# Kernel tuning notes

Hardware: AMD Instinct MI355X
Metric: run time of the kernel (lower is better)

The kernel has to match this reference:

```python
import jax, jax.numpy as jnp
import numpy as np

D_H = 2048      # d_hidden
D_E = 1408      # d_expert (per routed expert)
E = 8           # n_routed_experts
K = 2           # n_experts_per_token (top-k)
N_SHARED = 2    # n_shared_experts -> shared expert dim = D_E * N_SHARED
B, S = 1, 2048
D_S = D_E * N_SHARED


def setup_inputs() -> dict:
    key = jax.random.key(0)
    ks = jax.random.split(key, 8)
    def init(k, shape, fan_in):
        # nn.Linear default init: U(-1/sqrt(fan_in), 1/sqrt(fan_in))
        bound = 1.0 / np.sqrt(fan_in)
        return jax.random.uniform(k, shape, jnp.float32, -bound, bound)
    x = jax.random.normal(ks[0], (B, S, D_H), jnp.float32)
    gate_W = init(ks[1], (E, D_H), D_H)          # router: logits = x @ gate_W.T
    Wg_e = init(ks[2], (E, D_E, D_H), D_H)       # per-expert W_gate (out,in)
    Wu_e = init(ks[3], (E, D_E, D_H), D_H)       # per-expert W_up
    Wd_e = init(ks[4], (E, D_H, D_E), D_E)       # per-expert W_down
    Wg_s = init(ks[5], (D_S, D_H), D_H)          # shared expert W_gate
    Wu_s = init(ks[6], (D_S, D_H), D_H)
    Wd_s = init(ks[7], (D_H, D_S), D_S)
    return {"x": x, "gate_W": gate_W, "Wg_e": Wg_e, "Wu_e": Wu_e,
            "Wd_e": Wd_e, "Wg_s": Wg_s, "Wu_s": Wu_s, "Wd_s": Wd_s}


def reference(x, gate_W, Wg_e, Wu_e, Wd_e, Wg_s, Wu_s, Wd_s):
    silu = jax.nn.silu
    # shared expert: SiLU-gated MLP over all tokens
    shared = (silu(x @ Wg_s.T) * (x @ Wu_s.T)) @ Wd_s.T          # [B,S,D_H]
    # gating: softmax over experts, then top-k scores/indices
    scores = jax.nn.softmax(x @ gate_W.T, axis=-1)                # [B,S,E]
    topk_scores, topk_idx = jax.lax.top_k(scores, K)              # [B,S,K]
    # dense combine weights w[t,e] = topk score if e selected else 0
    # (equivalent to the torch argsort-dispatch + scatter_reduce sum combine)
    w = jnp.sum(jax.nn.one_hot(topk_idx, E, dtype=x.dtype) * topk_scores[..., None], axis=-2)  # [B,S,E]
    xf = x.reshape(-1, D_H)                                       # [T,D_H], T = B*S
    wf = w.reshape(-1, E)                                         # [T,E]
    # per-expert SiLU-gated MLP, batched over experts
    g = jnp.einsum('td,efd->etf', xf, Wg_e)                       # [E,T,D_E]
    u = jnp.einsum('td,efd->etf', xf, Wu_e)
    h = silu(g) * u
    oe = jnp.einsum('etf,edf->etd', h, Wd_e)                      # [E,T,D_H]
    routed = jnp.einsum('etd,te->td', oe, wf).reshape(B, S, D_H)
    return routed + shared
```

## Files before the change

kernel.cpp:

```cpp
#include <hip/hip_runtime.h>

using short8 = __attribute__((ext_vector_type(8))) short;
using f32x4  = __attribute__((ext_vector_type(4))) float;
typedef unsigned short ushort_t;
typedef unsigned int u32;

#define T_TOK 2048
#define DH 2048
#define DE 1408
#define DS 2816
#define NB_GU 800
#define NB_DN 896

#define NGEc 23068672UL
#define NGSc 5767168UL
#define NXc  4194304UL
#define PA_CVT_BLOCKS 30208
#define PB_CVT_BLOCKS 14080

__device__ __forceinline__ unsigned short f2bf(float f) {
  unsigned u = __float_as_uint(f);
  u += 0x7FFF + ((u >> 16) & 1);
  return (unsigned short)(u >> 16);
}

__device__ __forceinline__ void gl_lds16(const void* g, void* l) {
  __builtin_amdgcn_global_load_lds((const __attribute__((address_space(1))) u32*)g,
                                   (__attribute__((address_space(3))) u32*)l, 16, 0, 0);
}

__device__ __forceinline__ short8 pack_bf8(float4 a, float4 b) {
  short8 o;
  o[0] = (short)f2bf(a.x); o[1] = (short)f2bf(a.y);
  o[2] = (short)f2bf(a.z); o[3] = (short)f2bf(a.w);
  o[4] = (short)f2bf(b.x); o[5] = (short)f2bf(b.y);
  o[6] = (short)f2bf(b.z); o[7] = (short)f2bf(b.w);
  return o;
}

__global__ void phaseA_kernel(const float* __restrict__ x, const float* __restrict__ gW,
                              int* __restrict__ counts, int* __restrict__ tok_e,
                              int* __restrict__ tok_slot, float* __restrict__ tok_w,
                              const float* __restrict__ Wg_e, const float* __restrict__ Wu_e,
                              const float* __restrict__ Wg_s, const float* __restrict__ Wu_s,
                              ushort_t* wbg_e, ushort_t* wbu_e,
                              ushort_t* wbg_s, ushort_t* wbu_s, ushort_t* xb) {
  int b = blockIdx.x;
  int tid = threadIdx.x;
  if (b < 512) {
    int wid = tid >> 6, lane = tid & 63;
    int t = b * 4 + wid;
    float acc[8] = {0.f,0.f,0.f,0.f,0.f,0.f,0.f,0.f};
    const float* xt = x + (size_t)t * DH;
    for (int i = lane; i < DH; i += 64) {
      float xv = xt[i];
#pragma unroll
      for (int e = 0; e < 8; e++) acc[e] += xv * gW[e * DH + i];
    }
#pragma unroll
    for (int e = 0; e < 8; e++) {
#pragma unroll
      for (int off = 32; off > 0; off >>= 1) acc[e] += __shfl_xor(acc[e], off);
    }
    if (lane == 0) {
      float mx = acc[0];
      for (int e = 1; e < 8; e++) mx = fmaxf(mx, acc[e]);
      float p[8], se = 0.f;
      for (int e = 0; e < 8; e++) { p[e] = __expf(acc[e] - mx); se += p[e]; }
      for (int e = 0; e < 8; e++) p[e] /= se;
      int i1 = 0;
      for (int e = 1; e < 8; e++) if (p[e] > p[i1]) i1 = e;
      int i2 = (i1 == 0) ? 1 : 0;
      for (int e = 0; e < 8; e++) if (e != i1 && p[e] > p[i2]) i2 = e;
      int s1 = atomicAdd(&counts[i1], 1);
      int s2 = atomicAdd(&counts[i2], 1);
      tok_e[2 * t] = i1;     tok_e[2 * t + 1] = i2;
      tok_slot[2 * t] = s1;  tok_slot[2 * t + 1] = s2;
      tok_w[2 * t] = p[i1];  tok_w[2 * t + 1] = p[i2];
    }
    return;
  }
  size_t i = (size_t)(b - 512) * 2048 + (size_t)tid * 8;
  const float* s; ushort_t* d; size_t o;
  if      (i < NGEc)                    { s = Wg_e; d = wbg_e; o = i; }
  else if (i < 2 * NGEc)                { s = Wu_e; d = wbu_e; o = i - NGEc; }
  else if (i < 2 * NGEc + NGSc)         { s = Wg_s; d = wbg_s; o = i - 2 * NGEc; }
  else if (i < 2 * NGEc + 2 * NGSc)     { s = Wu_s; d = wbu_s; o = i - 2 * NGEc - NGSc; }
  else                                  { s = x;    d = xb;    o = i - 2 * NGEc - 2 * NGSc; }
  float4 a = *(const float4*)(s + o);
  float4 bb = *(const float4*)(s + o + 4);
  *(short8*)(d + o) = pack_bf8(a, bb);
}

__global__ void prefix_assign_kernel(const int* __restrict__ counts, int* __restrict__ ebase,
                                     int* __restrict__ gu_off, int* __restrict__ dn_off,
                                     const int* __restrict__ tok_e, int* __restrict__ tok_slot,
                                     int* __restrict__ slot2tok) {
  __shared__ int sbase[8];
  if (threadIdx.x == 0) {
    int a = 0;
    for (int e = 0; e < 8; e++) { sbase[e] = a; ebase[e] = a; a += counts[e]; }
    int g = 0, d = 0;
    for (int z = 0; z < 8; z++) {
      gu_off[z] = g; dn_off[z] = d;
      int L = (counts[z] + 127) >> 7;
      g += L * 11; d += L * 16;
    }
    gu_off[8] = g; g += 176;
    gu_off[9] = g; g += 176;
    gu_off[10] = g;
    dn_off[8] = d; d += 256;
    dn_off[9] = d;
  }
  __syncthreads();
  for (int idx = threadIdx.x; idx < T_TOK * 2; idx += blockDim.x) {
    int e = tok_e[idx];
    int g = sbase[e] + tok_slot[idx];
    tok_slot[idx] = g;
    slot2tok[g] = idx >> 1;
  }
}

#define GU_BK 32
#define GU_OP 8192
#define GU_BUF 24576
__global__ __launch_bounds__(256, 2) void phaseB_kernel(
    const ushort_t* __restrict__ xb, const int* __restrict__ counts,
    const int* __restrict__ ebase, const int* __restrict__ gu_off,
    const int* __restrict__ slot2tok,
    const ushort_t* __restrict__ Wbg_e, const ushort_t* __restrict__ Wbu_e,
    const ushort_t* __restrict__ Wbg_s, const ushort_t* __restrict__ Wbu_s,
    ushort_t* __restrict__ h_r, ushort_t* __restrict__ h_s,
    const float* __restrict__ Wd_e, const float* __restrict__ Wd_s,
    ushort_t* wbd_e, ushort_t* wbd_s) {
  __shared__ char smem[2 * GU_BUF];
  int tid = threadIdx.x;
  if (blockIdx.x >= NB_GU) {
    size_t i = (size_t)(blockIdx.x - NB_GU) * 2048 + (size_t)tid * 8;
    const float* s; ushort_t* d; size_t o;
    if (i < NGEc) { s = Wd_e; d = wbd_e; o = i; }
    else          { s = Wd_s; d = wbd_s; o = i - NGEc; }
    float4 a = *(const float4*)(s + o);
    float4 bb = *(const float4*)(s + o + 4);
    *(short8*)(d + o) = pack_bf8(a, bb);
    return;
  }
  int b = blockIdx.x;
  int c = (b & 7) * (NB_GU >> 3) + (b >> 3);
  int off[11];
#pragma unroll
  for (int zz = 0; zz < 11; zz++) off[zz] = gu_off[zz];
  if (c >= off[10]) return;
  int z = 0;
#pragma unroll
  for (int zz = 1; zz < 10; zz++) if (c >= off[zz]) z = zz;
  int cz = c - off[z];

  bool routed = (z < 8);
  int cnt, gbase, Lm;
  const ushort_t *Bg, *Bu;
  if (routed) {
    cnt = counts[z]; gbase = ebase[z];
    Lm = (cnt + 127) >> 7;
    Bg = Wbg_e + (size_t)z * DE * DH;
    Bu = Wbu_e + (size_t)z * DE * DH;
  } else {
    cnt = T_TOK; gbase = 0; Lm = 16;
    Bg = Wbg_s + (size_t)(z - 8) * 1408 * DH;
    Bu = Wbu_s + (size_t)(z - 8) * 1408 * DH;
  }
  int mt = cz % Lm, y = cz / Lm;
  int m0 = mt * 128, n0 = y * 128;

  int lane = tid & 63, w = tid >> 6;
  int lr = lane & 15, lk = lane >> 4;
  int wr = w >> 1, wc = w & 1;

  const ushort_t* asrc[2];
  const ushort_t* gsrc[2];
  const ushort_t* usrc[2];
  int dst[2];
#pragma unroll
  for (int j = 0; j < 2; j++) {
    int r = (w * 2 + j) * 16 + (lane >> 2);
    int lrow = m0 + r;
    int tok = routed ? ((lrow < cnt) ? slot2tok[gbase + lrow] : 0) : lrow;
    int cs = (lane & 3) ^ ((r >> 1) & 3);
    asrc[j] = xb + (size_t)tok * DH + cs * 8;
    gsrc[j] = Bg + (size_t)(n0 + r) * DH + cs * 8;
    usrc[j] = Bu + (size_t)(n0 + r) * DH + cs * 8;
    dst[j] = (w * 2 + j) * 1024;
  }

  f32x4 accg[4][4] = {};
  f32x4 accu[4][4] = {};

#define GU_STAGE(buf, k0)                                              \
  {                                                                    \
    char* bb = smem + (buf) * GU_BUF;                                  \
    _Pragma("unroll")                                                  \
    for (int j = 0; j < 2; j++) {                                      \
      gl_lds16(asrc[j] + (k0), bb + dst[j]);                           \
      gl_lds16(gsrc[j] + (k0), bb + GU_OP + dst[j]);                   \
      gl_lds16(usrc[j] + (k0), bb + 2 * GU_OP + dst[j]);               \
    }                                                                  \
  }

  GU_STAGE(0, 0);
  __syncthreads();
  int cur = 0;
  for (int kc = 0; kc < DH; kc += GU_BK) {
    if (kc + GU_BK < DH) GU_STAGE(cur ^ 1, kc + GU_BK);
    const char* bb = smem + cur * GU_BUF;
    short8 af[4], bg[4], bu[4];
#pragma unroll
    for (int m = 0; m < 4; m++) {
      int rr = wr * 64 + m * 16 + lr;
      af[m] = *(const short8*)(bb + rr * 64 + ((lk ^ ((rr >> 1) & 3)) << 4));
    }
#pragma unroll
    for (int n = 0; n < 4; n++) {
      int cc = wc * 64 + n * 16 + lr;
      bg[n] = *(const short8*)(bb + GU_OP + cc * 64 + ((lk ^ ((cc >> 1) & 3)) << 4));
      bu[n] = *(const short8*)(bb + 2 * GU_OP + cc * 64 + ((lk ^ ((cc >> 1) & 3)) << 4));
    }
#pragma unroll
    for (int m = 0; m < 4; m++) {
#pragma unroll
      for (int n = 0; n < 4; n++) {
        accg[m][n] = __builtin_amdgcn_mfma_f32_16x16x32_bf16(af[m], bg[n], accg[m][n], 0, 0, 0);
        accu[m][n] = __builtin_amdgcn_mfma_f32_16x16x32_bf16(af[m], bu[n], accu[m][n], 0, 0, 0);
      }
    }
    __syncthreads();
    cur ^= 1;
  }
#pragma unroll
  for (int m = 0; m < 4; m++) {
    int rowl = m0 + wr * 64 + m * 16 + lk * 4;
#pragma unroll
    for (int n = 0; n < 4; n++) {
      int col = n0 + wc * 64 + n * 16 + lr;
#pragma unroll
      for (int j = 0; j < 4; j++) {
        float g = accg[m][n][j], u = accu[m][n][j];
        float s = g / (1.f + __expf(-g));
        unsigned short hv = f2bf(s * u);
        if (routed) {
          if (rowl + j < cnt) h_r[(size_t)(gbase + rowl + j) * DE + col] = hv;
        } else {
          h_s[(size_t)(rowl + j) * DS + (z - 8) * 1408 + col] = hv;
        }
      }
    }
  }
}

#define DN_BK 32
#define DN_OP 8192
#define DN_BUF 16384
__global__ __launch_bounds__(256, 3) void down_kernel(
    const ushort_t* __restrict__ h_r, const ushort_t* __restrict__ h_s,
    const int* __restrict__ counts, const int* __restrict__ ebase,
    const int* __restrict__ dn_off,
    const ushort_t* __restrict__ Wbd_e, const ushort_t* __restrict__ Wbd_s,
    float* __restrict__ oe, float* __restrict__ out) {
  __shared__ char smem[3 * DN_BUF];

  int b = blockIdx.x;
  int c = (b & 7) * (NB_DN >> 3) + (b >> 3);
  int off[10];
#pragma unroll
  for (int zz = 0; zz < 10; zz++) off[zz] = dn_off[zz];
  if (c >= off[9]) return;
  int z = 0;
#pragma unroll
  for (int zz = 1; zz < 9; zz++) if (c >= off[zz]) z = zz;
  int cz = c - off[z];

  bool routed = (z < 8);
  int cnt, gbase, K, Lm;
  const ushort_t* Abase;
  const ushort_t* B;
  if (routed) {
    cnt = counts[z]; gbase = ebase[z];
    Lm = (cnt + 127) >> 7;
    K = DE;
    Abase = h_r + (size_t)gbase * DE;
    B = Wbd_e + (size_t)z * DH * DE;
  } else {
    cnt = T_TOK; gbase = 0; Lm = 16;
    K = DS;
    Abase = h_s;
    B = Wbd_s;
  }
  int mt = cz % Lm, y = cz / Lm;
  int m0 = mt * 128, n0 = y * 128;

  int tid = threadIdx.x;
  int lane = tid & 63, w = tid >> 6;
  int lr = lane & 15, lk = lane >> 4;
  int wr = w >> 1, wc = w & 1;

  const ushort_t* asrc[2];
  const ushort_t* bsrc[2];
  int dst[2];
#pragma unroll
  for (int j = 0; j < 2; j++) {
    int r = (w * 2 + j) * 16 + (lane >> 2);
    int cs = (lane & 3) ^ ((r >> 1) & 3);
    asrc[j] = Abase + (size_t)(m0 + r) * K + cs * 8;
    bsrc[j] = B + (size_t)(n0 + r) * K + cs * 8;
    dst[j] = (w * 2 + j) * 1024;
  }

  f32x4 acc[4][4] = {};

#define DN_STAGE(sbuf, k0)                                            \
  {                                                                   \
    char* bb = smem + (sbuf) * DN_BUF;                                \
    _Pragma("unroll")                                                 \
    for (int j = 0; j < 2; j++) {                                     \
      gl_lds16(asrc[j] + (k0), bb + dst[j]);                          \
      gl_lds16(bsrc[j] + (k0), bb + DN_OP + dst[j]);                  \
    }                                                                 \
  }

  const int NT = K / DN_BK;
  DN_STAGE(0, 0);
  DN_STAGE(1, DN_BK);
  int cur = 0;
  for (int i = 0; i < NT; i++) {
    if (i + 1 < NT) asm volatile("s_waitcnt vmcnt(4)" ::: "memory");
    else            asm volatile("s_waitcnt vmcnt(0)" ::: "memory");
    __builtin_amdgcn_s_barrier();
    asm volatile("" ::: "memory");
    if (i + 2 < NT) {
      int s2 = cur + 2; if (s2 >= 3) s2 -= 3;
      DN_STAGE(s2, (i + 2) * DN_BK);
    }
    const char* bb = smem + cur * DN_BUF;
    short8 af[4], bf[4];
#pragma unroll
    for (int m = 0; m < 4; m++) {
      int rr = wr * 64 + m * 16 + lr;
      af[m] = *(const short8*)(bb + rr * 64 + ((lk ^ ((rr >> 1) & 3)) << 4));
    }
#pragma unroll
    for (int n = 0; n < 4; n++) {
      int cc = wc * 64 + n * 16 + lr;
      bf[n] = *(const short8*)(bb + DN_OP + cc * 64 + ((lk ^ ((cc >> 1) & 3)) << 4));
    }
#pragma unroll
    for (int m = 0; m < 4; m++) {
#pragma unroll
      for (int n = 0; n < 4; n++) {
        acc[m][n] = __builtin_amdgcn_mfma_f32_16x16x32_bf16(af[m], bf[n], acc[m][n], 0, 0, 0);
      }
    }
    cur = (cur + 1 >= 3) ? 0 : cur + 1;
  }
#pragma unroll
  for (int m = 0; m < 4; m++) {
    int rowl = m0 + wr * 64 + m * 16 + lk * 4;
#pragma unroll
    for (int n = 0; n < 4; n++) {
      int col = n0 + wc * 64 + n * 16 + lr;
#pragma unroll
      for (int j = 0; j < 4; j++) {
        if (routed) {
          if (rowl + j < cnt) oe[(size_t)(gbase + rowl + j) * DH + col] = acc[m][n][j];
        } else {
          out[(size_t)(rowl + j) * DH + col] = acc[m][n][j];
        }
      }
    }
  }
}

__global__ void combine_kernel(const int* __restrict__ tok_gslot,
                               const float* __restrict__ tok_w,
                               const float* __restrict__ oe,
                               float* __restrict__ out) {
  int t = blockIdx.x;
  int g1 = tok_gslot[2 * t], g2 = tok_gslot[2 * t + 1];
  float w1 = tok_w[2 * t], w2 = tok_w[2 * t + 1];
  int i = threadIdx.x * 8;
  const float4* p1 = (const float4*)(oe + (size_t)g1 * DH + i);
  const float4* p2 = (const float4*)(oe + (size_t)g2 * DH + i);
  float4* po = (float4*)(out + (size_t)t * DH + i);
  float4 a0 = p1[0], a1 = p1[1];
  float4 b0 = p2[0], b1 = p2[1];
  float4 o0 = po[0], o1 = po[1];
  o0.x += w1 * a0.x + w2 * b0.x;  o0.y += w1 * a0.y + w2 * b0.y;
  o0.z += w1 * a0.z + w2 * b0.z;  o0.w += w1 * a0.w + w2 * b0.w;
  o1.x += w1 * a1.x + w2 * b1.x;  o1.y += w1 * a1.y + w2 * b1.y;
  o1.z += w1 * a1.z + w2 * b1.z;  o1.w += w1 * a1.w + w2 * b1.w;
  po[0] = o0; po[1] = o1;
}

extern "C" void kernel_launch(void* const* d_in, const int* in_sizes, int n_in,
                              void* d_out, int out_size, void* d_ws, size_t ws_size,
                              hipStream_t stream) {
  const float* x    = (const float*)d_in[0];
  const float* gW   = (const float*)d_in[1];
  const float* Wg_e = (const float*)d_in[2];
  const float* Wu_e = (const float*)d_in[3];
  const float* Wd_e = (const float*)d_in[4];
  const float* Wg_s = (const float*)d_in[5];
  const float* Wu_s = (const float*)d_in[6];
  const float* Wd_s = (const float*)d_in[7];
  float* out = (float*)d_out;

  char* ws = (char*)d_ws;
  int*   counts   = (int*)ws;
  int*   ebase    = (int*)(ws + 64);
  int*   gu_off   = (int*)(ws + 128);
  int*   dn_off   = (int*)(ws + 192);
  int*   tok_e    = (int*)(ws + 256);
  int*   tok_slot = (int*)(ws + 256 + 16384);
  float* tok_w    = (float*)(ws + 256 + 32768);
  int*   slot2tok = (int*)(ws + 256 + 49152);
  ushort_t* xb  = (ushort_t*)(ws + 131072);
  ushort_t* h_r = (ushort_t*)(ws + 131072 + (size_t)T_TOK * DH * 2);
  ushort_t* h_s = h_r + (size_t)4096 * DE;
  float*    oe  = (float*)((char*)h_s + (size_t)T_TOK * DS * 2);
  ushort_t* wb  = (ushort_t*)((char*)oe + (size_t)4096 * DH * 4);
  ushort_t* wbg_e = wb;
  ushort_t* wbu_e = wb + NGEc;
  ushort_t* wbd_e = wb + 2 * NGEc;
  ushort_t* wbg_s = wb + 3 * NGEc;
  ushort_t* wbu_s = wbg_s + NGSc;
  ushort_t* wbd_s = wbg_s + 2 * NGSc;

  hipMemsetAsync(counts, 0, 64, stream);
  phaseA_kernel<<<512 + PA_CVT_BLOCKS, 256, 0, stream>>>(
      x, gW, counts, tok_e, tok_slot, tok_w,
      Wg_e, Wu_e, Wg_s, Wu_s, wbg_e, wbu_e, wbg_s, wbu_s, xb);
  prefix_assign_kernel<<<1, 256, 0, stream>>>(counts, ebase, gu_off, dn_off,
                                              tok_e, tok_slot, slot2tok);
  phaseB_kernel<<<NB_GU + PB_CVT_BLOCKS, 256, 0, stream>>>(
      xb, counts, ebase, gu_off, slot2tok, wbg_e, wbu_e, wbg_s, wbu_s, h_r, h_s,
      Wd_e, Wd_s, wbd_e, wbd_s);
  down_kernel<<<NB_DN, 256, 0, stream>>>(
      h_r, h_s, counts, ebase, dn_off, wbd_e, wbd_s, oe, out);
  combine_kernel<<<T_TOK, 256, 0, stream>>>(tok_slot, tok_w, oe, out);
}
```

Before: 389.1 us.

## Enlarge down-projection tiles to 256x256 with 512-thread blocks and BK=64

The down-projection GEMM moves from 128x128 tiles with 256 threads and a triple-buffered BK=32 pipeline to 256x256 tiles with 512 threads, BK=64 double buffering in 128KB of dynamic LDS, and an XOR swizzle. The tile schedule in prefix_assign is updated to match, and the grid drops to 256 blocks, about one per CU. The goal is higher operand reuse and less global traffic per FLOP. In exchange, occupancy falls to one block per CU, padding waste on routed experts grows, and a full barrier is taken each K step.

```diff
diff --git a/kernel.cpp b/kernel.cpp
--- a/kernel.cpp
+++ b/kernel.cpp
@@ -10,11 +10,10 @@
 #define DE 1408
 #define DS 2816
 #define NB_GU 800
-#define NB_DN 896
+#define DN_NB 256
 
 #define NGEc 23068672UL
 #define NGSc 5767168UL
-#define NXc  4194304UL
 #define PA_CVT_BLOCKS 30208
 #define PB_CVT_BLOCKS 14080
 
@@ -104,12 +103,14 @@
     for (int z = 0; z < 8; z++) {
       gu_off[z] = g; dn_off[z] = d;
       int L = (counts[z] + 127) >> 7;
-      g += L * 11; d += L * 16;
+      g += L * 11;
+      int Ld = (counts[z] + 255) >> 8;
+      d += Ld * 8;
     }
     gu_off[8] = g; g += 176;
     gu_off[9] = g; g += 176;
     gu_off[10] = g;
-    dn_off[8] = d; d += 256;
+    dn_off[8] = d; d += 64;
     dn_off[9] = d;
   }
   __syncthreads();
@@ -256,19 +257,16 @@
   }
 }
 
-#define DN_BK 32
-#define DN_OP 8192
-#define DN_BUF 16384
-__global__ __launch_bounds__(256, 3) void down_kernel(
+__global__ __launch_bounds__(512, 1) void down_kernel(
     const ushort_t* __restrict__ h_r, const ushort_t* __restrict__ h_s,
     const int* __restrict__ counts, const int* __restrict__ ebase,
     const int* __restrict__ dn_off,
     const ushort_t* __restrict__ Wbd_e, const ushort_t* __restrict__ Wbd_s,
     float* __restrict__ oe, float* __restrict__ out) {
-  __shared__ char smem[3 * DN_BUF];
+  extern __shared__ char smem[];
 
   int b = blockIdx.x;
-  int c = (b & 7) * (NB_DN >> 3) + (b >> 3);
+  int c = (b & 7) * (DN_NB >> 3) + (b >> 3);
   int off[10];
 #pragma unroll
   for (int zz = 0; zz < 10; zz++) off[zz] = dn_off[zz];
@@ -281,91 +279,103 @@
   bool routed = (z < 8);
   int cnt, gbase, K, Lm;
   const ushort_t* Abase;
-  const ushort_t* B;
+  const ushort_t* Bw;
   if (routed) {
     cnt = counts[z]; gbase = ebase[z];
-    Lm = (cnt + 127) >> 7;
+    Lm = (cnt + 255) >> 8;
     K = DE;
     Abase = h_r + (size_t)gbase * DE;
-    B = Wbd_e + (size_t)z * DH * DE;
+    Bw = Wbd_e + (size_t)z * DH * DE;
   } else {
-    cnt = T_TOK; gbase = 0; Lm = 16;
+    cnt = T_TOK; gbase = 0; Lm = 8;
     K = DS;
     Abase = h_s;
-    B = Wbd_s;
+    Bw = Wbd_s;
   }
   int mt = cz % Lm, y = cz / Lm;
-  int m0 = mt * 128, n0 = y * 128;
+  int m0 = mt * 256, n0 = y * 256;
 
   int tid = threadIdx.x;
   int lane = tid & 63, w = tid >> 6;
   int lr = lane & 15, lk = lane >> 4;
-  int wr = w >> 1, wc = w & 1;
-
-  const ushort_t* asrc[2];
-  const ushort_t* bsrc[2];
-  int dst[2];
-#pragma unroll
-  for (int j = 0; j < 2; j++) {
-    int r = (w * 2 + j) * 16 + (lane >> 2);
-    int cs = (lane & 3) ^ ((r >> 1) & 3);
+  int wm = w >> 2, wn = w & 3;
+
+  const ushort_t* asrc[4];
+  const ushort_t* bsrc[4];
+  int dst4[4];
+#pragma unroll
+  for (int j = 0; j < 4; j++) {
+    int r = (w * 4 + j) * 8 + (lane >> 3);
+    int cs = (lane & 7) ^ (r & 7);
     asrc[j] = Abase + (size_t)(m0 + r) * K + cs * 8;
-    bsrc[j] = B + (size_t)(n0 + r) * K + cs * 8;
-    dst[j] = (w * 2 + j) * 1024;
-  }
-
-  f32x4 acc[4][4] = {};
-
-#define DN_STAGE(sbuf, k0)                                            \
+    bsrc[j] = Bw + (size_t)(n0 + r) * K + cs * 8;
+    dst4[j] = (w * 4 + j) * 1024;
+  }
+
+  f32x4 acc[8][4] = {};
+
+#define DN_STAGE(buf, k0)                                             \
   {                                                                   \
-    char* bb = smem + (sbuf) * DN_BUF;                                \
+    char* ab = smem + (buf) * 32768;                                  \
+    char* wb2 = smem + 65536 + (buf) * 32768;                         \
     _Pragma("unroll")                                                 \
-    for (int j = 0; j < 2; j++) {                                     \
-      gl_lds16(asrc[j] + (k0), bb + dst[j]);                          \
-      gl_lds16(bsrc[j] + (k0), bb + DN_OP + dst[j]);                  \
+    for (int j = 0; j < 4; j++) {                                     \
+      gl_lds16(asrc[j] + (k0), ab + dst4[j]);                         \
+      gl_lds16(bsrc[j] + (k0), wb2 + dst4[j]);                        \
     }                                                                 \
   }
 
-  const int NT = K / DN_BK;
+  const int nt = K >> 6;
   DN_STAGE(0, 0);
-  DN_STAGE(1, DN_BK);
+  __syncthreads();
   int cur = 0;
-  for (int i = 0; i < NT; i++) {
-    if (i + 1 < NT) asm volatile("s_waitcnt vmcnt(4)" ::: "memory");
-    else            asm volatile("s_waitcnt vmcnt(0)" ::: "memory");
-    __builtin_amdgcn_s_barrier();
-    asm volatile("" ::: "memory");
-    if (i + 2 < NT) {
-      int s2 = cur + 2; if (s2 >= 3) s2 -= 3;
-      DN_STAGE(s2, (i + 2) * DN_BK);
-    }
-    const char* bb = smem + cur * DN_BUF;
-    short8 af[4], bf[4];
-#pragma unroll
-    for (int m = 0; m < 4; m++) {
-      int rr = wr * 64 + m * 16 + lr;
-      af[m] = *(const short8*)(bb + rr * 64 + ((lk ^ ((rr >> 1) & 3)) << 4));
-    }
+  for (int t = 0; t < nt; t++) {
+    if (t + 1 < nt) DN_STAGE(cur ^ 1, (t + 1) * 64);
+    const char* ab = smem + cur * 32768;
+    const char* wb2 = smem + 65536 + cur * 32768;
+    short8 bf[4][2];
 #pragma unroll
     for (int n = 0; n < 4; n++) {
-      int cc = wc * 64 + n * 16 + lr;
-      bf[n] = *(const short8*)(bb + DN_OP + cc * 64 + ((lk ^ ((cc >> 1) & 3)) << 4));
-    }
-#pragma unroll
-    for (int m = 0; m < 4; m++) {
-#pragma unroll
-      for (int n = 0; n < 4; n++) {
-        acc[m][n] = __builtin_amdgcn_mfma_f32_16x16x32_bf16(af[m], bf[n], acc[m][n], 0, 0, 0);
-      }
-    }
-    cur = (cur + 1 >= 3) ? 0 : cur + 1;
-  }
-#pragma unroll
-  for (int m = 0; m < 4; m++) {
-    int rowl = m0 + wr * 64 + m * 16 + lk * 4;
+#pragma unroll
+      for (int ks = 0; ks < 2; ks++) {
+        int cc = wn * 64 + n * 16 + lr;
+        bf[n][ks] = *(const short8*)(wb2 + cc * 128 + ((ks * 64 + lk * 16) ^ ((cc & 7) << 4)));
+      }
+    }
+    __builtin_amdgcn_s_setprio(1);
+#pragma unroll
+    for (int mh = 0; mh < 2; mh++) {
+      short8 af[4][2];
+#pragma unroll
+      for (int m4 = 0; m4 < 4; m4++) {
+#pragma unroll
+        for (int ks = 0; ks < 2; ks++) {
+          int rr = wm * 128 + (mh * 4 + m4) * 16 + lr;
+          af[m4][ks] = *(const short8*)(ab + rr * 128 + ((ks * 64 + lk * 16) ^ ((rr & 7) << 4)));
+        }
+      }
+#pragma unroll
+      for (int m4 = 0; m4 < 4; m4++) {
+#pragma unroll
+        for (int n = 0; n < 4; n++) {
+#pragma unroll
+          for (int ks = 0; ks < 2; ks++) {
+            acc[mh * 4 + m4][n] = __builtin_amdgcn_mfma_f32_16x16x32_bf16(
+                af[m4][ks], bf[n][ks], acc[mh * 4 + m4][n], 0, 0, 0);
+          }
+        }
+      }
+    }
+    __builtin_amdgcn_s_setprio(0);
+    __syncthreads();
+    cur ^= 1;
+  }
+#pragma unroll
+  for (int m = 0; m < 8; m++) {
+    int rowl = m0 + wm * 128 + m * 16 + lk * 4;
 #pragma unroll
     for (int n = 0; n < 4; n++) {
-      int col = n0 + wc * 64 + n * 16 + lr;
+      int col = n0 + wn * 64 + n * 16 + lr;
 #pragma unroll
       for (int j = 0; j < 4; j++) {
         if (routed) {
@@ -433,6 +443,9 @@
   ushort_t* wbu_s = wbg_s + NGSc;
   ushort_t* wbd_s = wbg_s + 2 * NGSc;
 
+  hipFuncSetAttribute((const void*)down_kernel,
+                      hipFuncAttributeMaxDynamicSharedMemorySize, 131072);
+
   hipMemsetAsync(counts, 0, 64, stream);
   phaseA_kernel<<<512 + PA_CVT_BLOCKS, 256, 0, stream>>>(
       x, gW, counts, tok_e, tok_slot, tok_w,
@@ -442,7 +455,7 @@
   phaseB_kernel<<<NB_GU + PB_CVT_BLOCKS, 256, 0, stream>>>(
       xb, counts, ebase, gu_off, slot2tok, wbg_e, wbu_e, wbg_s, wbu_s, h_r, h_s,
       Wd_e, Wd_s, wbd_e, wbd_s);
-  down_kernel<<<NB_DN, 256, 0, stream>>>(
+  down_kernel<<<DN_NB, 512, 131072, stream>>>(
       h_r, h_s, counts, ebase, dn_off, wbd_e, wbd_s, oe, out);
   combine_kernel<<<T_TOK, 256, 0, stream>>>(tok_slot, tok_w, oe, out);
 }
```

Measured after the change: 363.0 us. 6.7% less time.
